# Performance work log

Measured on AMD Instinct MI355X. Metric: run time of the kernel, lower is better.

The kernel has to match this reference:

```python
import jax, jax.numpy as jnp
import numpy as np

N = 50000
E = 800000
IN_C = 128
HID = 128
HEADS = 4
NEG_SLOPE = 0.2


def setup_inputs() -> dict:
    key = jax.random.key(0)
    ks = jax.random.split(key, 10)
    out_c = HID // HEADS  # 32
    glorot = lambda k, shape: jax.random.normal(k, shape, jnp.float32) * np.sqrt(2.0 / (shape[0] + shape[-1]))
    return {
        "x": jax.random.normal(ks[0], (N, IN_C), jnp.float32),
        "edge_index": jax.random.randint(ks[1], (2, E), 0, N, jnp.int64),
        # layer 1: GATConv(IN_C, out_c, heads=4, concat=True)
        "W1": glorot(ks[2], (IN_C, HEADS * out_c)),
        "att_src1": glorot(ks[3], (HEADS, out_c)),
        "att_dst1": glorot(ks[4], (HEADS, out_c)),
        "b1": jnp.zeros((HID,), jnp.float32),
        # layer 2: GATConv(HID, HID, heads=1, concat=False)
        "W2": glorot(ks[5], (HID, HID)),
        "att_src2": glorot(ks[6], (1, HID)),
        "att_dst2": glorot(ks[7], (1, HID)),
        "b2": jnp.zeros((HID,), jnp.float32),
    }


def _gat_conv(x, src, dst, W, att_src, att_dst, bias, heads, out_c):
    n = x.shape[0]
    h = (x @ W).reshape(n, heads, out_c)                 # [N, H, C]
    a_src = jnp.einsum("nhc,hc->nh", h, att_src)          # [N, H]
    a_dst = jnp.einsum("nhc,hc->nh", h, att_dst)          # [N, H]
    e = jax.nn.leaky_relu(a_src[src] + a_dst[dst], NEG_SLOPE)  # [E, H]
    # segment softmax over incoming edges of each dst node
    m = jax.ops.segment_max(e, dst, num_segments=n)
    p = jnp.exp(e - m[dst])
    denom = jax.ops.segment_sum(p, dst, num_segments=n)
    alpha = p / (denom[dst] + 1e-16)                      # [E, H]
    msg = h[src] * alpha[:, :, None]                      # [E, H, C]
    out = jax.ops.segment_sum(msg, dst, num_segments=n)   # [N, H, C]
    return out.reshape(n, heads * out_c) + bias


def reference(x, edge_index, W1, att_src1, att_dst1, b1, W2, att_src2, att_dst2, b2):
    n = x.shape[0]
    # PyG GATConv default add_self_loops=True
    loop = jnp.arange(n, dtype=edge_index.dtype)
    src = jnp.concatenate([edge_index[0], loop])
    dst = jnp.concatenate([edge_index[1], loop])

    out_c = HID // HEADS
    h = _gat_conv(x, src, dst, W1, att_src1, att_dst1, b1, HEADS, out_c)
    h = jax.nn.elu(h)  # dropout is identity in eval mode
    out = _gat_conv(h, src, dst, W2, att_src2, att_dst2, b2, 1, HID)
    return out
```

## Files before the change

kernel.cpp:

```cpp
#include <hip/hip_runtime.h>
#include <hip/hip_bf16.h>
#include <math.h>


#define NEG_SLOPE 0.2f
#define NBLK 256

using bf16x8 = __attribute__((ext_vector_type(8))) short;
using f32x4  = __attribute__((ext_vector_type(4))) float;

__device__ inline unsigned short f2bf(float x) {
    union { float f; unsigned int u; } v; v.f = x;
    unsigned int b = v.u + 0x7fffu + ((v.u >> 16) & 1u);
    return (unsigned short)(b >> 16);
}
__device__ inline unsigned int pack2bf(float a, float b) {
    return (unsigned int)f2bf(a) | ((unsigned int)f2bf(b) << 16);
}
__device__ inline float bf_lo(unsigned int u) { return __uint_as_float(u << 16); }
__device__ inline float bf_hi(unsigned int u) { return __uint_as_float(u & 0xffff0000u); }

__device__ inline int excl_scan_256(int v, int* scratch4) {
    const int t = threadIdx.x, lane = t & 63, w = t >> 6;
    int incl = v;
#pragma unroll
    for (int o = 1; o < 64; o <<= 1) {
        int u = __shfl_up(incl, o, 64);
        if (lane >= o) incl += u;
    }
    if (lane == 63) scratch4[w] = incl;
    __syncthreads();
    int wb = 0;
#pragma unroll
    for (int k = 0; k < 4; ++k)
        if (k < w) wb += scratch4[k];
    __syncthreads();
    return wb + incl - v;
}

__global__ __launch_bounds__(256) void part_hist(const int* __restrict__ ei,
                                                 int* __restrict__ hist,
                                                 int E, int NB, int epb) {
    __shared__ int h[256];
    const int t = threadIdx.x;
    h[t] = 0;
    __syncthreads();
    const int e0 = blockIdx.x * epb;
    const int e1 = min(e0 + epb, E);
    for (int e = e0 + t; e < e1; e += 256) atomicAdd(&h[ei[E + e] >> 8], 1);
    __syncthreads();
    if (t < NB) hist[t * NBLK + blockIdx.x] = h[t];
}

__global__ __launch_bounds__(256) void part_scan(int* __restrict__ hist,
                                                 int* __restrict__ btotal) {
    __shared__ int s4[4];
    const int b = blockIdx.x, t = threadIdx.x;
    const int v = hist[b * NBLK + t];
    const int ex = excl_scan_256(v, s4);
    hist[b * NBLK + t] = ex;
    if (t == 255) btotal[b] = ex + v;
}

__global__ __launch_bounds__(256) void part_scatter(const int* __restrict__ ei,
                                                    const int* __restrict__ hist,
                                                    const int* __restrict__ btotal,
                                                    unsigned int* __restrict__ part,
                                                    int E, int NB, int epb) {
    __shared__ int s4[4];
    __shared__ int cur[256];
    const int t = threadIdx.x;
    const int tv = (t < NB) ? btotal[t] : 0;
    const int pb = excl_scan_256(tv, s4);
    cur[t] = (t < NB) ? pb + hist[t * NBLK + blockIdx.x] : 0;
    __syncthreads();
    const int e0 = blockIdx.x * epb;
    const int e1 = min(e0 + epb, E);
    for (int e = e0 + t; e < e1; e += 256) {
        const int d = ei[E + e];
        const int s = ei[e];
        const int pos = atomicAdd(&cur[d >> 8], 1);
        part[pos] = (unsigned int)s | ((unsigned int)(d & 255) << 16);
    }
}

__global__ __launch_bounds__(256) void csr_build(const unsigned int* __restrict__ part,
                                                 const int* __restrict__ btotal,
                                                 int* __restrict__ offs,
                                                 int* __restrict__ csr,
                                                 int n, int NB, int E) {
    __shared__ int s4[4];
    __shared__ int cnt[256], curq[256];
    __shared__ int sPB, sPE, sCB;
    const int b = blockIdx.x, t = threadIdx.x;
    const int tv = (t < NB) ? btotal[t] : 0;
    const int nnt = (t < NB) ? max(0, min(256, n - t * 256)) : 0;
    const int e1 = excl_scan_256(tv, s4);
    const int e2 = excl_scan_256(tv + nnt, s4);
    if (t == b) { sPB = e1; sPE = e1 + tv; sCB = e2; }
    const int node = b * 256 + t;
    cnt[t] = (node < n) ? 1 : 0;
    __syncthreads();
    for (int i = sPB + t; i < sPE; i += 256) atomicAdd(&cnt[(part[i] >> 16) & 255], 1);
    __syncthreads();
    const int c = cnt[t];
    const int loc = excl_scan_256(c, s4);
    curq[t] = loc + ((node < n) ? 1 : 0);
    if (node < n) {
        offs[node] = sCB + loc;
        csr[sCB + loc] = node;
    }
    if (b == 0 && t == 0) offs[n] = E + n;
    __syncthreads();
    for (int i = sPB + t; i < sPE; i += 256) {
        const unsigned int u = part[i];
        const int pos = atomicAdd(&curq[(u >> 16) & 255], 1);
        csr[sCB + pos] = (int)(u & 0xffffu);
    }
}

__global__ __launch_bounds__(256) void prep_w(const float* __restrict__ W1,
                                              const float* __restrict__ W2,
                                              unsigned short* __restrict__ WT1,
                                              unsigned short* __restrict__ WT2) {
    const float* W = blockIdx.x ? W2 : W1;
    unsigned short* WT = blockIdx.x ? WT2 : WT1;
    __shared__ float Wl[64][132];
    const int tid = threadIdx.x;
    for (int p = 0; p < 2; ++p) {
        if (p) __syncthreads();
        for (int u = tid; u < 2048; u += 256) {
            int row = u >> 5, ch = u & 31;
            float4 v = *(const float4*)(W + (size_t)(p * 64 + row) * 128 + ch * 4);
            Wl[row][ch * 4 + 0] = v.x; Wl[row][ch * 4 + 1] = v.y;
            Wl[row][ch * 4 + 2] = v.z; Wl[row][ch * 4 + 3] = v.w;
        }
        __syncthreads();
        for (int u = tid; u < 2048; u += 256) {
            int c = u >> 4, kc = u & 15;
            uint2 o;
            o.x = pack2bf(Wl[kc * 4 + 0][c], Wl[kc * 4 + 1][c]);
            o.y = pack2bf(Wl[kc * 4 + 2][c], Wl[kc * 4 + 3][c]);
            *(uint2*)(WT + (size_t)c * 128 + p * 64 + kc * 4) = o;
        }
    }
}

template <int H, bool IN_F32>
__global__ __launch_bounds__(256) void gemm_att(const float* __restrict__ Xf,
                                                const unsigned short* __restrict__ Xb,
                                                const unsigned short* __restrict__ WTb,
                                                unsigned int* __restrict__ Yb,
                                                const float* __restrict__ att_s,
                                                const float* __restrict__ att_d,
                                                float* __restrict__ as_,
                                                float* __restrict__ ad_, int n) {
    __shared__ unsigned short XL[64 * 128];
    __shared__ unsigned short WL[128 * 128];
    const int tid = threadIdx.x;
    const int r0g = blockIdx.x * 64;
#pragma unroll
    for (int p = 0; p < 4; ++p) {
        int u = tid + 256 * p;
        int row = u >> 4, ch = u & 15;
        uint4 v = {0, 0, 0, 0};
        int gr = r0g + row;
        if (gr < n) {
            if constexpr (IN_F32) {
                const float4* xp = (const float4*)(Xf + (size_t)gr * 128 + ch * 8);
                float4 f0 = xp[0], f1 = xp[1];
                v.x = pack2bf(f0.x, f0.y); v.y = pack2bf(f0.z, f0.w);
                v.z = pack2bf(f1.x, f1.y); v.w = pack2bf(f1.z, f1.w);
            } else {
                v = *(const uint4*)(Xb + (size_t)gr * 128 + ch * 8);
            }
        }
        int byte = (ch * 16) ^ ((row & 7) << 4);
        *(uint4*)((char*)XL + row * 256 + byte) = v;
    }
#pragma unroll
    for (int p = 0; p < 8; ++p) {
        int u = tid + 256 * p;
        int c = u >> 4, ch = u & 15;
        uint4 v = *(const uint4*)(WTb + (size_t)c * 128 + ch * 8);
        int byte = (ch * 16) ^ ((c & 7) << 4);
        *(uint4*)((char*)WL + c * 256 + byte) = v;
    }
    __syncthreads();

    const int w = tid >> 6, lane = tid & 63;
    const int lr = lane & 15, lq = lane >> 4;
    const int swz = (lr & 7) << 4;
    f32x4 acc[8];
#pragma unroll
    for (int cf = 0; cf < 8; ++cf) acc[cf] = (f32x4){0.f, 0.f, 0.f, 0.f};

    const char* XB = (const char*)XL + (w * 16 + lr) * 256;
    const char* WB = (const char*)WL + lr * 256;
#pragma unroll
    for (int k4 = 0; k4 < 4; ++k4) {
        const int off = (k4 * 64 + lq * 16) ^ swz;
        bf16x8 a = *(const bf16x8*)(XB + off);
#pragma unroll
        for (int cf = 0; cf < 8; ++cf) {
            bf16x8 b = *(const bf16x8*)(WB + cf * 4096 + off);
            acc[cf] = __builtin_amdgcn_mfma_f32_16x16x32_bf16(a, b, acc[cf], 0, 0, 0);
        }
    }

#pragma unroll
    for (int r = 0; r < 4; ++r) {
        int grow = r0g + w * 16 + lq * 4 + r;
        if (grow < n) {
            uint4 o;
            o.x = pack2bf(acc[0][r], acc[1][r]);
            o.y = pack2bf(acc[2][r], acc[3][r]);
            o.z = pack2bf(acc[4][r], acc[5][r]);
            o.w = pack2bf(acc[6][r], acc[7][r]);
            *(uint4*)((unsigned short*)Yb + (size_t)grow * 128 + lr * 8) = o;
        }
    }

    if constexpr (H == 4) {
        float pa[4][4], pd[4][4];
#pragma unroll
        for (int h = 0; h < 4; ++h)
#pragma unroll
            for (int r = 0; r < 4; ++r) { pa[h][r] = 0.f; pd[h][r] = 0.f; }
#pragma unroll
        for (int cf = 0; cf < 8; ++cf) {
            const float ws = att_s[cf * 16 + lr];
            const float wd = att_d[cf * 16 + lr];
            constexpr int dummy = 0; (void)dummy;
#pragma unroll
            for (int r = 0; r < 4; ++r) {
                pa[cf >> 1][r] = fmaf(acc[cf][r], ws, pa[cf >> 1][r]);
                pd[cf >> 1][r] = fmaf(acc[cf][r], wd, pd[cf >> 1][r]);
            }
        }
#pragma unroll
        for (int o = 1; o < 16; o <<= 1) {
#pragma unroll
            for (int h = 0; h < 4; ++h)
#pragma unroll
                for (int r = 0; r < 4; ++r) {
                    pa[h][r] += __shfl_xor(pa[h][r], o, 64);
                    pd[h][r] += __shfl_xor(pd[h][r], o, 64);
                }
        }
        const int h = lr & 3, r = lr >> 2;
        float va = 0.f, vd = 0.f;
#pragma unroll
        for (int hh = 0; hh < 4; ++hh)
#pragma unroll
            for (int rr = 0; rr < 4; ++rr)
                if (h == hh && r == rr) { va = pa[hh][rr]; vd = pd[hh][rr]; }
        const int node = r0g + w * 16 + lq * 4 + r;
        if (node < n) {
            as_[(size_t)node * 4 + h] = va;
            ad_[(size_t)node * 4 + h] = vd;
        }
    } else {
        float pa[4], pd[4];
#pragma unroll
        for (int r = 0; r < 4; ++r) { pa[r] = 0.f; pd[r] = 0.f; }
#pragma unroll
        for (int cf = 0; cf < 8; ++cf) {
            const float ws = att_s[cf * 16 + lr];
            const float wd = att_d[cf * 16 + lr];
#pragma unroll
            for (int r = 0; r < 4; ++r) {
                pa[r] = fmaf(acc[cf][r], ws, pa[r]);
                pd[r] = fmaf(acc[cf][r], wd, pd[r]);
            }
        }
#pragma unroll
        for (int o = 1; o < 16; o <<= 1) {
#pragma unroll
            for (int r = 0; r < 4; ++r) {
                pa[r] += __shfl_xor(pa[r], o, 64);
                pd[r] += __shfl_xor(pd[r], o, 64);
            }
        }
        const int r = lr & 3;
        float va = 0.f, vd = 0.f;
#pragma unroll
        for (int rr = 0; rr < 4; ++rr)
            if (r == rr) { va = pa[rr]; vd = pd[rr]; }
        const int node = r0g + w * 16 + lq * 4 + r;
        if (node < n && lr < 8) {
            if (lr < 4) as_[node] = va;
            else        ad_[node] = vd;
        }
    }
}

template <int H, bool DO_ELU, bool OUT_BF16>
__global__ __launch_bounds__(256) void gat_gather4(
    const int* __restrict__ csr, const int* __restrict__ offs,
    const float* __restrict__ as_, const float* __restrict__ ad_,
    const unsigned int* __restrict__ hb,
    const float* __restrict__ bias, float* __restrict__ outf,
    unsigned short* __restrict__ outb, int n)
{
    constexpr int PW = (H == 4) ? 8 : 2;
    __shared__ float plds[4][64][PW];
    const int node = (int)(((size_t)blockIdx.x * blockDim.x + threadIdx.x) >> 6);
    if (node >= n) return;
    const int lane = threadIdx.x & 63;
    const int w = threadIdx.x >> 6;
    const int hd = lane & 3;
    const int col0 = ((2 * lane) & 7) * 16 + (lane >> 2);
    const int col1 = col0 + 16;
    const int start = offs[node];
    const int deg = offs[node + 1] - start;

    float adx = 0.f, ady = 0.f, adz = 0.f, adw = 0.f;
    if constexpr (H == 4) {
        const float4 adv = *(const float4*)(ad_ + (size_t)node * 4);
        adx = adv.x; ady = adv.y; adz = adv.z; adw = adv.w;
    } else {
        adx = ad_[node];
    }

    float2 acc = {0.f, 0.f};
    float dsx = 0.f, dsy = 0.f, dsz = 0.f, dsw = 0.f;

    for (int base = 0; base < deg; base += 64) {
        const int cnt = min(deg - base, 64);
        if (lane < cnt) {
            const int s = csr[start + base + lane];
            const float sf = __int_as_float(s);
            if constexpr (H == 4) {
                const float4 a = ((const float4*)as_)[s];
                float e0 = a.x + adx; e0 = fmaxf(e0, NEG_SLOPE * e0);
                float e1 = a.y + ady; e1 = fmaxf(e1, NEG_SLOPE * e1);
                float e2 = a.z + adz; e2 = fmaxf(e2, NEG_SLOPE * e2);
                float e3 = a.w + adw; e3 = fmaxf(e3, NEG_SLOPE * e3);
                float4 p4 = {__expf(e0), __expf(e1), __expf(e2), __expf(e3)};
                dsx += p4.x; dsy += p4.y; dsz += p4.z; dsw += p4.w;
                *(float4*)&plds[w][lane][0] = p4;
                float4 s4 = {sf, sf, sf, sf};
                *(float4*)&plds[w][lane][4] = s4;
            } else {
                float e0 = as_[s] + adx; e0 = fmaxf(e0, NEG_SLOPE * e0);
                float p = __expf(e0);
                dsx += p;
                float2 ps = {p, sf};
                *(float2*)&plds[w][lane][0] = ps;
            }
        }
        asm volatile("s_waitcnt lgkmcnt(0)" ::: "memory");
        __builtin_amdgcn_sched_barrier(0);

        float pA = 0.f, pB = 0.f, pC = 0.f;
        unsigned int hA = 0, hB = 0, hC = 0;
#define PRELB(S, T)                                                             \
    if ((T) < cnt) {                                                            \
        const float* q = &plds[w][(T)][0];                                      \
        int _s;                                                                 \
        if constexpr (H == 4) { p##S = q[hd]; _s = __float_as_int(q[4 + hd]); } \
        else                  { p##S = q[0];  _s = __float_as_int(q[1]); }      \
        h##S = hb[(size_t)(unsigned)_s * 64 + lane];                            \
    }
#define CONSB(S)                                                                \
    {                                                                           \
        acc.x = fmaf(p##S, bf_lo(h##S), acc.x);                                 \
        acc.y = fmaf(p##S, bf_hi(h##S), acc.y);                                 \
    }
        PRELB(A, 0)
        PRELB(B, 1)
        PRELB(C, 2)
        int t = 0;
        for (; t + 3 <= cnt; t += 3) {
            CONSB(A) PRELB(A, t + 3)
            CONSB(B) PRELB(B, t + 4)
            CONSB(C) PRELB(C, t + 5)
        }
        if (t < cnt)     CONSB(A)
        if (t + 1 < cnt) CONSB(B)
        if (t + 2 < cnt) CONSB(C)
#undef PRELB
#undef CONSB
    }

#pragma unroll
    for (int o = 1; o < 64; o <<= 1) {
        dsx += __shfl_xor(dsx, o, 64);
        if constexpr (H == 4) {
            dsy += __shfl_xor(dsy, o, 64);
            dsz += __shfl_xor(dsz, o, 64);
            dsw += __shfl_xor(dsw, o, 64);
        }
    }
    float ds;
    if constexpr (H == 4) ds = hd == 0 ? dsx : hd == 1 ? dsy : hd == 2 ? dsz : dsw;
    else                  ds = dsx;

    const float bvx = bias[col0], bvy = bias[col1];
    const float inv = 1.f / (ds + 1e-16f);
    float v0 = acc.x * inv + bvx;
    float v1 = acc.y * inv + bvy;
    if constexpr (DO_ELU) {
        v0 = v0 > 0.f ? v0 : __expf(v0) - 1.f;
        v1 = v1 > 0.f ? v1 : __expf(v1) - 1.f;
    }
    if constexpr (OUT_BF16) {
        unsigned short* o16 = outb + (size_t)node * 128;
        o16[col0] = f2bf(v0);
        o16[col1] = f2bf(v1);
    } else {
        float* o32 = outf + (size_t)node * 128;
        o32[col0] = v0;
        o32[col1] = v1;
    }
}

extern "C" void kernel_launch(void* const* d_in, const int* in_sizes, int n_in,
                              void* d_out, int out_size, void* d_ws, size_t ws_size,
                              hipStream_t stream) {
    const float* x        = (const float*)d_in[0];
    const int*   ei       = (const int*)d_in[1];
    const float* W1       = (const float*)d_in[2];
    const float* att_src1 = (const float*)d_in[3];
    const float* att_dst1 = (const float*)d_in[4];
    const float* b1       = (const float*)d_in[5];
    const float* W2       = (const float*)d_in[6];
    const float* att_src2 = (const float*)d_in[7];
    const float* att_dst2 = (const float*)d_in[8];
    const float* b2       = (const float*)d_in[9];

    const int n  = in_sizes[0] / 128;
    const int E  = in_sizes[1] / 2;
    const int ET = E + n;
    const int NB = (n + 255) >> 8;
    const int epb = (E + NBLK - 1) / NBLK;

    unsigned int*   ws32 = (unsigned int*)d_ws;
    unsigned int*   Yb   = ws32;
    unsigned int*   Bb   = Yb + (size_t)n * 64;
    unsigned short* WT1  = (unsigned short*)(Bb + (size_t)n * 64);
    unsigned short* WT2  = WT1 + 128 * 128;
    float*          as_  = (float*)(WT2 + 128 * 128);
    float*          ad_  = as_ + (size_t)n * 4;
    int*            offs = (int*)(ad_ + (size_t)n * 4);
    int*            csr  = offs + n + 1;
    unsigned int*   part = (unsigned int*)(csr + ET);
    int*            hist = (int*)(part + E);
    int*            btot = hist + (size_t)NB * NBLK;

    float* outf = (float*)d_out;

    part_hist<<<NBLK, 256, 0, stream>>>(ei, hist, E, NB, epb);
    part_scan<<<NB, 256, 0, stream>>>(hist, btot);
    part_scatter<<<NBLK, 256, 0, stream>>>(ei, hist, btot, part, E, NB, epb);
    csr_build<<<NB, 256, 0, stream>>>(part, btot, offs, csr, n, NB, E);

    prep_w<<<2, 256, 0, stream>>>(W1, W2, WT1, WT2);

    gemm_att<4, true><<<(n + 63) / 64, 256, 0, stream>>>(
        x, nullptr, WT1, Yb, att_src1, att_dst1, as_, ad_, n);
    gat_gather4<4, true, true><<<((size_t)n * 64 + 255) / 256, 256, 0, stream>>>(
        csr, offs, as_, ad_, Yb, b1, nullptr, (unsigned short*)Bb, n);

    gemm_att<1, false><<<(n + 63) / 64, 256, 0, stream>>>(
        nullptr, (const unsigned short*)Bb, WT2, Yb, att_src2, att_dst2, as_, ad_, n);
    gat_gather4<1, false, false><<<((size_t)n * 64 + 255) / 256, 256, 0, stream>>>(
        csr, offs, as_, ad_, Yb, b2, outf, nullptr, n);
}
```

Baseline: 233.7 us.

## Fuse weight prep into histogram kernel, enlarge GEMM tiles, streamline gather addressing

```diff
diff --git a/kernel.cpp b/kernel.cpp
--- a/kernel.cpp
+++ b/kernel.cpp
@@ -38,11 +38,38 @@
     return wb + incl - v;
 }
 
-__global__ __launch_bounds__(256) void part_hist(const int* __restrict__ ei,
-                                                 int* __restrict__ hist,
-                                                 int E, int NB, int epb) {
+__global__ __launch_bounds__(256) void part_hist_prep(const int* __restrict__ ei,
+                                                      int* __restrict__ hist,
+                                                      int E, int NB, int epb,
+                                                      const float* __restrict__ W1,
+                                                      const float* __restrict__ W2,
+                                                      unsigned short* __restrict__ WT1,
+                                                      unsigned short* __restrict__ WT2) {
+    const int t = threadIdx.x;
+    if (blockIdx.x >= NBLK) {
+        __shared__ float Wl[64][132];
+        const float* W = (blockIdx.x - NBLK) ? W2 : W1;
+        unsigned short* WT = (blockIdx.x - NBLK) ? WT2 : WT1;
+        for (int p = 0; p < 2; ++p) {
+            if (p) __syncthreads();
+            for (int u = t; u < 2048; u += 256) {
+                int row = u >> 5, ch = u & 31;
+                float4 v = *(const float4*)(W + (size_t)(p * 64 + row) * 128 + ch * 4);
+                Wl[row][ch * 4 + 0] = v.x; Wl[row][ch * 4 + 1] = v.y;
+                Wl[row][ch * 4 + 2] = v.z; Wl[row][ch * 4 + 3] = v.w;
+            }
+            __syncthreads();
+            for (int u = t; u < 2048; u += 256) {
+                int c = u >> 4, kc = u & 15;
+                uint2 o;
+                o.x = pack2bf(Wl[kc * 4 + 0][c], Wl[kc * 4 + 1][c]);
+                o.y = pack2bf(Wl[kc * 4 + 2][c], Wl[kc * 4 + 3][c]);
+                *(uint2*)(WT + (size_t)c * 128 + p * 64 + kc * 4) = o;
+            }
+        }
+        return;
+    }
     __shared__ int h[256];
-    const int t = threadIdx.x;
     h[t] = 0;
     __syncthreads();
     const int e0 = blockIdx.x * epb;
@@ -119,35 +146,8 @@
     }
 }
 
-__global__ __launch_bounds__(256) void prep_w(const float* __restrict__ W1,
-                                              const float* __restrict__ W2,
-                                              unsigned short* __restrict__ WT1,
-                                              unsigned short* __restrict__ WT2) {
-    const float* W = blockIdx.x ? W2 : W1;
-    unsigned short* WT = blockIdx.x ? WT2 : WT1;
-    __shared__ float Wl[64][132];
-    const int tid = threadIdx.x;
-    for (int p = 0; p < 2; ++p) {
-        if (p) __syncthreads();
-        for (int u = tid; u < 2048; u += 256) {
-            int row = u >> 5, ch = u & 31;
-            float4 v = *(const float4*)(W + (size_t)(p * 64 + row) * 128 + ch * 4);
-            Wl[row][ch * 4 + 0] = v.x; Wl[row][ch * 4 + 1] = v.y;
-            Wl[row][ch * 4 + 2] = v.z; Wl[row][ch * 4 + 3] = v.w;
-        }
-        __syncthreads();
-        for (int u = tid; u < 2048; u += 256) {
-            int c = u >> 4, kc = u & 15;
-            uint2 o;
-            o.x = pack2bf(Wl[kc * 4 + 0][c], Wl[kc * 4 + 1][c]);
-            o.y = pack2bf(Wl[kc * 4 + 2][c], Wl[kc * 4 + 3][c]);
-            *(uint2*)(WT + (size_t)c * 128 + p * 64 + kc * 4) = o;
-        }
-    }
-}
-
 template <int H, bool IN_F32>
-__global__ __launch_bounds__(256) void gemm_att(const float* __restrict__ Xf,
+__global__ __launch_bounds__(512) void gemm_att(const float* __restrict__ Xf,
                                                 const unsigned short* __restrict__ Xb,
                                                 const unsigned short* __restrict__ WTb,
                                                 unsigned int* __restrict__ Yb,
@@ -155,13 +155,13 @@
                                                 const float* __restrict__ att_d,
                                                 float* __restrict__ as_,
                                                 float* __restrict__ ad_, int n) {
-    __shared__ unsigned short XL[64 * 128];
+    __shared__ unsigned short XL[128 * 128];
     __shared__ unsigned short WL[128 * 128];
     const int tid = threadIdx.x;
-    const int r0g = blockIdx.x * 64;
+    const int r0g = blockIdx.x * 128;
 #pragma unroll
     for (int p = 0; p < 4; ++p) {
-        int u = tid + 256 * p;
+        int u = tid + 512 * p;
         int row = u >> 4, ch = u & 15;
         uint4 v = {0, 0, 0, 0};
         int gr = r0g + row;
@@ -179,8 +179,8 @@
         *(uint4*)((char*)XL + row * 256 + byte) = v;
     }
 #pragma unroll
-    for (int p = 0; p < 8; ++p) {
-        int u = tid + 256 * p;
+    for (int p = 0; p < 4; ++p) {
+        int u = tid + 512 * p;
         int c = u >> 4, ch = u & 15;
         uint4 v = *(const uint4*)(WTb + (size_t)c * 128 + ch * 8);
         int byte = (ch * 16) ^ ((c & 7) << 4);
@@ -231,7 +231,6 @@
         for (int cf = 0; cf < 8; ++cf) {
             const float ws = att_s[cf * 16 + lr];
             const float wd = att_d[cf * 16 + lr];
-            constexpr int dummy = 0; (void)dummy;
 #pragma unroll
             for (int r = 0; r < 4; ++r) {
                 pa[cf >> 1][r] = fmaf(acc[cf][r], ws, pa[cf >> 1][r]);
@@ -296,7 +295,7 @@
 }
 
 template <int H, bool DO_ELU, bool OUT_BF16>
-__global__ __launch_bounds__(256) void gat_gather4(
+__global__ __launch_bounds__(256) void gat_gather5(
     const int* __restrict__ csr, const int* __restrict__ offs,
     const float* __restrict__ as_, const float* __restrict__ ad_,
     const unsigned int* __restrict__ hb,
@@ -304,16 +303,24 @@
     unsigned short* __restrict__ outb, int n)
 {
     constexpr int PW = (H == 4) ? 8 : 2;
-    __shared__ float plds[4][64][PW];
+    __shared__ float plds[4][68][PW];
     const int node = (int)(((size_t)blockIdx.x * blockDim.x + threadIdx.x) >> 6);
     if (node >= n) return;
     const int lane = threadIdx.x & 63;
     const int w = threadIdx.x >> 6;
     const int hd = lane & 3;
+    const int lane4 = lane * 4;
     const int col0 = ((2 * lane) & 7) * 16 + (lane >> 2);
     const int col1 = col0 + 16;
     const int start = offs[node];
     const int deg = offs[node + 1] - start;
+    const char* hbp = (const char*)hb;
+    const char* pb = (const char*)&plds[w][0][0] + ((H == 4) ? hd * 8 : 0);
+
+    if (lane < 3) {
+#pragma unroll
+        for (int k = 0; k < PW; ++k) plds[w][64 + lane][k] = 0.f;
+    }
 
     float adx = 0.f, ady = 0.f, adz = 0.f, adw = 0.f;
     if constexpr (H == 4) {
@@ -328,23 +335,28 @@
 
     for (int base = 0; base < deg; base += 64) {
         const int cnt = min(deg - base, 64);
-        if (lane < cnt) {
-            const int s = csr[start + base + lane];
-            const float sf = __int_as_float(s);
+        {
+            const bool act = lane < cnt;
+            const int s = act ? csr[start + base + lane] : 0;
+            const float sf = __int_as_float(s << 8);
             if constexpr (H == 4) {
                 const float4 a = ((const float4*)as_)[s];
                 float e0 = a.x + adx; e0 = fmaxf(e0, NEG_SLOPE * e0);
                 float e1 = a.y + ady; e1 = fmaxf(e1, NEG_SLOPE * e1);
                 float e2 = a.z + adz; e2 = fmaxf(e2, NEG_SLOPE * e2);
                 float e3 = a.w + adw; e3 = fmaxf(e3, NEG_SLOPE * e3);
-                float4 p4 = {__expf(e0), __expf(e1), __expf(e2), __expf(e3)};
-                dsx += p4.x; dsy += p4.y; dsz += p4.z; dsw += p4.w;
-                *(float4*)&plds[w][lane][0] = p4;
-                float4 s4 = {sf, sf, sf, sf};
-                *(float4*)&plds[w][lane][4] = s4;
+                float p0 = act ? __expf(e0) : 0.f;
+                float p1 = act ? __expf(e1) : 0.f;
+                float p2 = act ? __expf(e2) : 0.f;
+                float p3 = act ? __expf(e3) : 0.f;
+                dsx += p0; dsy += p1; dsz += p2; dsw += p3;
+                float4 w0 = {p0, sf, p1, sf};
+                float4 w1 = {p2, sf, p3, sf};
+                *(float4*)&plds[w][lane][0] = w0;
+                *(float4*)&plds[w][lane][4] = w1;
             } else {
                 float e0 = as_[s] + adx; e0 = fmaxf(e0, NEG_SLOPE * e0);
-                float p = __expf(e0);
+                float p = act ? __expf(e0) : 0.f;
                 dsx += p;
                 float2 ps = {p, sf};
                 *(float2*)&plds[w][lane][0] = ps;
@@ -353,20 +365,18 @@
         asm volatile("s_waitcnt lgkmcnt(0)" ::: "memory");
         __builtin_amdgcn_sched_barrier(0);
 
-        float pA = 0.f, pB = 0.f, pC = 0.f;
-        unsigned int hA = 0, hB = 0, hC = 0;
-#define PRELB(S, T)                                                             \
-    if ((T) < cnt) {                                                            \
-        const float* q = &plds[w][(T)][0];                                      \
-        int _s;                                                                 \
-        if constexpr (H == 4) { p##S = q[hd]; _s = __float_as_int(q[4 + hd]); } \
-        else                  { p##S = q[0];  _s = __float_as_int(q[1]); }      \
-        h##S = hb[(size_t)(unsigned)_s * 64 + lane];                            \
-    }
-#define CONSB(S)                                                                \
-    {                                                                           \
-        acc.x = fmaf(p##S, bf_lo(h##S), acc.x);                                 \
-        acc.y = fmaf(p##S, bf_hi(h##S), acc.y);                                 \
+        float pA, pB, pC;
+        unsigned int hA, hB, hC;
+#define PRELB(S, T)                                                              \
+    {                                                                            \
+        const float2 ps = *(const float2*)(pb + (size_t)(T) * (PW * 4));         \
+        p##S = ps.x;                                                             \
+        h##S = *(const unsigned int*)(hbp + (__float_as_int(ps.y) | lane4));     \
+    }
+#define CONSB(S)                                                                 \
+    {                                                                            \
+        acc.x = fmaf(p##S, bf_lo(h##S), acc.x);                                  \
+        acc.y = fmaf(p##S, bf_hi(h##S), acc.y);                                  \
     }
         PRELB(A, 0)
         PRELB(B, 1)
@@ -451,20 +461,19 @@
 
     float* outf = (float*)d_out;
 
-    part_hist<<<NBLK, 256, 0, stream>>>(ei, hist, E, NB, epb);
+    part_hist_prep<<<NBLK + 2, 256, 0, stream>>>(ei, hist, E, NB, epb,
+                                                 W1, W2, WT1, WT2);
     part_scan<<<NB, 256, 0, stream>>>(hist, btot);
     part_scatter<<<NBLK, 256, 0, stream>>>(ei, hist, btot, part, E, NB, epb);
     csr_build<<<NB, 256, 0, stream>>>(part, btot, offs, csr, n, NB, E);
 
-    prep_w<<<2, 256, 0, stream>>>(W1, W2, WT1, WT2);
-
-    gemm_att<4, true><<<(n + 63) / 64, 256, 0, stream>>>(
+    gemm_att<4, true><<<(n + 127) / 128, 512, 0, stream>>>(
         x, nullptr, WT1, Yb, att_src1, att_dst1, as_, ad_, n);
-    gat_gather4<4, true, true><<<((size_t)n * 64 + 255) / 256, 256, 0, stream>>>(
+    gat_gather5<4, true, true><<<((size_t)n * 64 + 255) / 256, 256, 0, stream>>>(
         csr, offs, as_, ad_, Yb, b1, nullptr, (unsigned short*)Bb, n);
 
-    gemm_att<1, false><<<(n + 63) / 64, 256, 0, stream>>>(
+    gemm_att<1, false><<<(n + 127) / 128, 512, 0, stream>>>(
         nullptr, (const unsigned short*)Bb, WT2, Yb, att_src2, att_dst2, as_, ad_, n);
-    gat_gather4<1, false, false><<<((size_t)n * 64 + 255) / 256, 256, 0, stream>>>(
+    gat_gather5<1, false, false><<<((size_t)n * 64 + 255) / 256, 256, 0, stream>>>(
         csr, offs, as_, ad_, Yb, b2, outf, nullptr, n);
 }
```

Result: slower. 240.7 us (+3.0%).
